# Kernel tuning notes

Measured on AMD Instinct MI355X. Metric: run time of the kernel, lower is better.

The kernel has to match this reference:

```python
import jax, jax.numpy as jnp
import numpy as np

N, K, CL, CP = 8192, 32, 384, 128   # residues, neighbours, local dim, pair dim
H, S, P = 4, 32, 8                   # heads, head size, query points


def setup_inputs() -> dict:
    key = jax.random.key(0)
    ks = jax.random.split(key, 12)

    def lin(k, fi, fo):
        return jax.random.normal(k, (fi, fo), jnp.float32) / jnp.sqrt(jnp.float32(fi))

    return {
        "local": jax.random.normal(ks[0], (N, CL), jnp.float32),
        "pair": jax.random.normal(ks[1], (N, K, CP), jnp.float32),
        "frames": jax.random.normal(ks[2], (N, 4, 4), jnp.float32),
        "neighbours": jax.random.randint(ks[3], (N, K), 0, N),
        "mask": jnp.ones((N, K), dtype=bool),
        "Wq": lin(ks[4], CL, H * S), "bq": jnp.zeros((H * S,), jnp.float32),
        "Wk": lin(ks[5], CL, S), "bk": jnp.zeros((S,), jnp.float32),
        "Wv": lin(ks[6], CL, S), "bv": jnp.zeros((S,), jnp.float32),
        "Wqp": lin(ks[7], CL, H * P * 3), "bqp": jnp.zeros((H * P * 3,), jnp.float32),
        "Wkp": lin(ks[8], CL, P * 3), "bkp": jnp.zeros((P * 3,), jnp.float32),
        "Wvp": lin(ks[9], CL, P * 3), "bvp": jnp.zeros((P * 3,), jnp.float32),
        "Wb": lin(ks[10], CP, H),
        "gamma": jnp.full((H,), np.log(np.exp(1.0) - 1.0), jnp.float32),
        "Wout": lin(ks[11], H * S + H * CP + H * P * 3, CL),
    }


def _ln(x):
    # hk.LayerNorm([-1], create_scale=False, create_offset=False), eps=1e-5
    m = x.mean(-1, keepdims=True)
    v = ((x - m) ** 2).mean(-1, keepdims=True)
    return (x - m) * jax.lax.rsqrt(v + 1e-5)


def reference(local, pair, frames, neighbours, mask,
              Wq, bq, Wk, bk, Wv, bv, Wqp, bqp, Wkp, bkp, Wvp, bvp,
              Wb, gamma, Wout):
    frames = frames.astype(jnp.float32)
    rot = frames[:, :3, :3]       # (N,3,3)
    trans = frames[:, :3, 3]      # (N,3)
    n = local.shape[0]

    q = _ln((local @ Wq + bq).reshape(n, H, S))   # (N,H,S)
    k = _ln(local @ Wk + bk)                      # (N,S)  single (shared) head
    v = local @ Wv + bv                           # (N,S)

    def pts(W, b, h):
        p = (local @ W + b).reshape(n, h, P, 3)
        # frames[:,None,None].apply_to_point: rot @ p + trans
        return jnp.einsum('nab,nhpb->nhpa', rot, p) + trans[:, None, None, :]

    qp = pts(Wqp, bqp, H)            # (N,H,P,3)
    kp = pts(Wkp, bkp, 1)[:, 0]      # (N,P,3)
    vp = pts(Wvp, bvp, 1)[:, 0]      # (N,P,3)

    w_C = jnp.sqrt(2.0 / (9.0 * P))
    w_L = jnp.sqrt(1.0 / 3.0)
    scale = jax.nn.softplus(gamma)[None, None, :] * w_C / 2   # (1,1,H)

    logits = jnp.einsum('nhc,nkc->nkh', q / jnp.sqrt(jnp.float32(S)), k[neighbours])
    diff = qp[:, None] - kp[neighbours][:, :, None]           # (N,K,H,P,3)
    dist = (diff ** 2).sum((-1, -2))                          # (N,K,H)
    logits = w_L * (logits - scale * dist + pair @ Wb)
    logits = jnp.where(mask[..., None], logits, -1e9)
    attn = jax.nn.softmax(logits, axis=1)
    attn = jnp.where(mask[..., None], attn, 0)

    local_up = jnp.einsum('nkh,nkc->nhc', attn, v[neighbours]).reshape(n, -1)
    pair_up = jnp.einsum('nkh,nkc->nhc', attn, pair).reshape(n, -1)
    pt = jnp.einsum('nkh,nkpa->nhpa', attn, vp[neighbours])   # (N,H,P,3)
    # apply_inverse_to_point: rot^T @ (x - trans)
    pt = jnp.einsum('nba,nhpb->nhpa', rot, pt - trans[:, None, None, :])

    result = jnp.concatenate([local_up, pair_up, pt.reshape(n, -1)], axis=-1)
    return result @ Wout
```

## Files before the change

### kernel.cpp

```cpp
#include <hip/hip_runtime.h>
#include <hip/hip_bf16.h>

#define NN 8192
#define KK 32
#define CL 384
#define CP 128
#define HH 4
#define SS 32
#define PP 8
#define PW 336
#define RW 736

__global__ void pack_weights(const float* __restrict__ Wq, const float* __restrict__ Wk,
                             const float* __restrict__ Wv, const float* __restrict__ Wqp,
                             const float* __restrict__ Wkp, const float* __restrict__ Wvp,
                             const float* __restrict__ bq, const float* __restrict__ bk,
                             const float* __restrict__ bv, const float* __restrict__ bqp,
                             const float* __restrict__ bkp, const float* __restrict__ bvp,
                             float* __restrict__ W_all, float* __restrict__ b_all) {
  int c = blockIdx.x;
  for (int j = threadIdx.x; j < PW; j += blockDim.x) {
    float w;
    if (j < 128)      w = Wq[c*128 + j];
    else if (j < 160) w = Wk[c*32 + (j-128)];
    else if (j < 192) w = Wv[c*32 + (j-160)];
    else if (j < 288) w = Wqp[c*96 + (j-192)];
    else if (j < 312) w = Wkp[c*24 + (j-288)];
    else              w = Wvp[c*24 + (j-312)];
    W_all[c*PW + j] = w;
    if (c == 0) {
      float b;
      if (j < 128)      b = bq[j];
      else if (j < 160) b = bk[j-128];
      else if (j < 192) b = bv[j-160];
      else if (j < 288) b = bqp[j-192];
      else if (j < 312) b = bkp[j-288];
      else              b = bvp[j-312];
      b_all[j] = b;
    }
  }
}

template<bool BIAS>
__global__ __launch_bounds__(256, 4) void gemm_f32(
    const float* __restrict__ A, const float* __restrict__ B,
    const float* __restrict__ bias, float* __restrict__ C,
    int M, int Kd, int Nc) {
  constexpr int BM = 64, BN = 64, BK = 32;
  __shared__ float As[BK][BM + 4];
  __shared__ float Bs[BK][BN + 4];
  int tid = threadIdx.x;
  int tx = tid & 15, ty = tid >> 4;
  int m0 = blockIdx.y * BM, n0 = blockIdx.x * BN;
  float acc[4][4] = {};
  for (int k0 = 0; k0 < Kd; k0 += BK) {
    int arow = tid >> 3, achunk = tid & 7;
#pragma unroll
    for (int half = 0; half < 2; ++half) {
      int m = arow + half * 32;
      float4 v = *(const float4*)(A + (size_t)(m0 + m) * Kd + k0 + achunk * 4);
      As[achunk*4+0][m] = v.x; As[achunk*4+1][m] = v.y;
      As[achunk*4+2][m] = v.z; As[achunk*4+3][m] = v.w;
    }
    int bc4 = tid & 15, br = tid >> 4;
#pragma unroll
    for (int half = 0; half < 2; ++half) {
      int kk = br + half * 16;
      float4 v = make_float4(0.f, 0.f, 0.f, 0.f);
      if (n0 + bc4 * 4 < Nc)
        v = *(const float4*)(B + (size_t)(k0 + kk) * Nc + n0 + bc4 * 4);
      *(float4*)&Bs[kk][bc4 * 4] = v;
    }
    __syncthreads();
#pragma unroll
    for (int kk = 0; kk < BK; ++kk) {
      float a[4], b[4];
      *(float4*)&a[0] = *(const float4*)&As[kk][ty * 4];
      *(float4*)&b[0] = *(const float4*)&Bs[kk][tx * 4];
#pragma unroll
      for (int i = 0; i < 4; ++i)
#pragma unroll
        for (int jj = 0; jj < 4; ++jj)
          acc[i][jj] += a[i] * b[jj];
    }
    __syncthreads();
  }
#pragma unroll
  for (int i = 0; i < 4; ++i) {
    int rowi = m0 + ty * 4 + i;
    int col = n0 + tx * 4;
    if (col + 3 < Nc) {
      float4 v;
      v.x = acc[i][0]; v.y = acc[i][1]; v.z = acc[i][2]; v.w = acc[i][3];
      if (BIAS) { v.x += bias[col]; v.y += bias[col+1]; v.z += bias[col+2]; v.w += bias[col+3]; }
      *(float4*)(C + (size_t)rowi * Nc + col) = v;
    } else {
      for (int jj = 0; jj < 4; ++jj) {
        int cc = col + jj;
        if (cc < Nc) C[(size_t)rowi * Nc + cc] = acc[i][jj] + (BIAS ? bias[cc] : 0.f);
      }
    }
  }
}

__global__ __launch_bounds__(256) void transform_kernel(
    const float* __restrict__ proj, const float* __restrict__ frames,
    float* __restrict__ feats) {
  int lane = threadIdx.x & 63;
  int node = blockIdx.x * 4 + (threadIdx.x >> 6);
  const float* pr = proj + (size_t)node * PW;
  float* fr = feats + (size_t)node * PW;
  const float* F = frames + (size_t)node * 16;
  int j = lane & 31;
#pragma unroll
  for (int pass = 0; pass < 2; ++pass) {
    int h = pass * 2 + (lane >> 5);
    float x = pr[h * 32 + j];
    float s = x;
#pragma unroll
    for (int m = 16; m >= 1; m >>= 1) s += __shfl_xor(s, m, 32);
    float mean = s * (1.f / 32.f);
    float d = x - mean;
    float vs = d * d;
#pragma unroll
    for (int m = 16; m >= 1; m >>= 1) vs += __shfl_xor(vs, m, 32);
    fr[h * 32 + j] = d / sqrtf(vs * (1.f / 32.f) + 1e-5f);
  }
  if (lane < 32) {
    float x = pr[128 + j];
    float s = x;
#pragma unroll
    for (int m = 16; m >= 1; m >>= 1) s += __shfl_xor(s, m, 32);
    float mean = s * (1.f / 32.f);
    float d = x - mean;
    float vs = d * d;
#pragma unroll
    for (int m = 16; m >= 1; m >>= 1) vs += __shfl_xor(vs, m, 32);
    fr[128 + j] = d / sqrtf(vs * (1.f / 32.f) + 1e-5f);
  } else {
    fr[160 + j] = pr[160 + j];
  }
  if (lane < 48) {
    int c = 192 + lane * 3;
    float x = pr[c], y = pr[c + 1], z = pr[c + 2];
#pragma unroll
    for (int a = 0; a < 3; ++a)
      fr[c + a] = F[a*4+0]*x + F[a*4+1]*y + F[a*4+2]*z + F[a*4+3];
  }
}

__global__ __launch_bounds__(256) void attn_kernel(
    const float* __restrict__ feats, const float* __restrict__ pair,
    const int* __restrict__ neighbours, const float* __restrict__ frames,
    const float* __restrict__ Wb, const float* __restrict__ gamma,
    float* __restrict__ result) {
  int n = blockIdx.x;
  int tid = threadIdx.x;
  __shared__ float qT_s[128];
  __shared__ float qp_s[96];
  __shared__ int   nb_s[32];
  __shared__ float kv_s[32][68];
  __shared__ float kpvp_s[32][52];
  __shared__ float pair_s[32][132];
  __shared__ float Wb_s[512];
  __shared__ float logit_s[32][4];
  __shared__ float attn_s[32][4];
  __shared__ float mred[4], sred[4];
  __shared__ float pt_s[96];

  const float* fr = feats + (size_t)n * PW;
  if (tid < 128) qT_s[(tid & 31) * 4 + (tid >> 5)] = fr[tid];
  if (tid < 96) qp_s[tid] = fr[192 + tid];
  if (tid < 32) nb_s[tid] = neighbours[n * KK + tid];
  Wb_s[tid] = Wb[tid];
  Wb_s[tid + 256] = Wb[tid + 256];
  __syncthreads();

  {
    int k = tid >> 3, r = tid & 7;
    const float* src = feats + (size_t)nb_s[k] * PW;
    float4 v0 = *(const float4*)(src + 128 + r * 8);
    float4 v1 = *(const float4*)(src + 128 + r * 8 + 4);
    *(float4*)&kv_s[k][r * 8] = v0;
    *(float4*)&kv_s[k][r * 8 + 4] = v1;
#pragma unroll
    for (int i = 0; i < 6; ++i) kpvp_s[k][r * 6 + i] = src[288 + r * 6 + i];
  }
  {
    const float* psrc = pair + (size_t)n * (KK * CP);
    for (int t = tid; t < 1024; t += 256) {
      int row = t >> 5, c4 = t & 31;
      float4 v = *(const float4*)(psrc + row * 128 + c4 * 4);
      *(float4*)&pair_s[row][c4 * 4] = v;
    }
  }
  __syncthreads();

  if (tid < 128) {
    int k = tid >> 2, h = tid & 3;
    float qk = 0.f;
#pragma unroll
    for (int c = 0; c < 32; ++c) qk += qT_s[c * 4 + h] * kv_s[k][c];
    float dist = 0.f;
#pragma unroll
    for (int r = 0; r < 24; ++r) {
      float d = qp_s[h * 24 + r] - kpvp_s[k][r];
      dist += d * d;
    }
    float bias = 0.f;
    for (int c = 0; c < 128; ++c) bias += pair_s[k][c] * Wb_s[c * 4 + h];
    float scale = log1pf(expf(gamma[h])) * (1.f / 6.f) * 0.5f;
    const float wL = 0.57735026918962576f;
    logit_s[k][h] = wL * (qk * 0.17677669529663687f - scale * dist + bias);
  }
  __syncthreads();
  if (tid < 4) {
    float m = -1e30f;
    for (int k = 0; k < 32; ++k) m = fmaxf(m, logit_s[k][tid]);
    float s = 0.f;
    for (int k = 0; k < 32; ++k) s += expf(logit_s[k][tid] - m);
    mred[tid] = m;
    sred[tid] = 1.f / s;
  }
  __syncthreads();
  if (tid < 128) {
    int k = tid >> 2, h = tid & 3;
    attn_s[k][h] = expf(logit_s[k][h] - mred[h]) * sred[h];
  }
  __syncthreads();

  float* out = result + (size_t)n * RW;
  if (tid < 128) {
    int h = tid >> 5, c = tid & 31;
    float s = 0.f;
#pragma unroll
    for (int k = 0; k < 32; ++k) s += attn_s[k][h] * kv_s[k][32 + c];
    out[h * 32 + c] = s;
  }
  if (tid < 96) {
    int h = tid / 24, r = tid % 24;
    float s = 0.f;
#pragma unroll
    for (int k = 0; k < 32; ++k) s += attn_s[k][h] * kpvp_s[k][24 + r];
    pt_s[tid] = s;
  }
#pragma unroll
  for (int half = 0; half < 2; ++half) {
    int idx = tid + half * 256;
    int h = idx >> 7, c = idx & 127;
    float s = 0.f;
#pragma unroll
    for (int k = 0; k < 32; ++k) s += attn_s[k][h] * pair_s[k][c];
    out[128 + h * 128 + c] = s;
  }
  __syncthreads();
  if (tid < 96) {
    int h = tid / 24, p = (tid % 24) / 3, a = tid % 3;
    const float* F = frames + (size_t)n * 16;
    float s = 0.f;
#pragma unroll
    for (int b = 0; b < 3; ++b)
      s += F[b * 4 + a] * (pt_s[h * 24 + p * 3 + b] - F[b * 4 + 3]);
    out[640 + tid] = s;
  }
}

extern "C" void kernel_launch(void* const* d_in, const int* in_sizes, int n_in,
                              void* d_out, int out_size, void* d_ws, size_t ws_size,
                              hipStream_t stream) {
  (void)in_sizes; (void)n_in; (void)out_size; (void)ws_size;
  const float* local      = (const float*)d_in[0];
  const float* pair       = (const float*)d_in[1];
  const float* frames     = (const float*)d_in[2];
  const int*   neighbours = (const int*)d_in[3];
  const float* Wq   = (const float*)d_in[5];
  const float* bq   = (const float*)d_in[6];
  const float* Wk   = (const float*)d_in[7];
  const float* bk   = (const float*)d_in[8];
  const float* Wv   = (const float*)d_in[9];
  const float* bv   = (const float*)d_in[10];
  const float* Wqp  = (const float*)d_in[11];
  const float* bqp  = (const float*)d_in[12];
  const float* Wkp  = (const float*)d_in[13];
  const float* bkp  = (const float*)d_in[14];
  const float* Wvp  = (const float*)d_in[15];
  const float* bvp  = (const float*)d_in[16];
  const float* Wb   = (const float*)d_in[17];
  const float* gamma= (const float*)d_in[18];
  const float* Wout = (const float*)d_in[19];

  float* ws     = (float*)d_ws;
  float* W_all  = ws;
  float* b_all  = W_all + 384 * PW;
  float* proj   = b_all + PW;
  float* feats  = proj + (size_t)NN * PW;
  float* result = feats + (size_t)NN * PW;
  float* out    = (float*)d_out;

  hipLaunchKernelGGL(pack_weights, dim3(CL), dim3(256), 0, stream,
                     Wq, Wk, Wv, Wqp, Wkp, Wvp, bq, bk, bv, bqp, bkp, bvp, W_all, b_all);
  hipLaunchKernelGGL((gemm_f32<true>), dim3((PW + 63) / 64, NN / 64), dim3(256), 0, stream,
                     local, W_all, b_all, proj, NN, CL, PW);
  hipLaunchKernelGGL(transform_kernel, dim3(NN / 4), dim3(256), 0, stream,
                     proj, frames, feats);
  hipLaunchKernelGGL(attn_kernel, dim3(NN), dim3(256), 0, stream,
                     feats, pair, neighbours, frames, Wb, gamma, result);
  hipLaunchKernelGGL((gemm_f32<false>), dim3(CL / 64, NN / 64), dim3(256), 0, stream,
                     result, Wout, nullptr, out, NN, RW, CL);
}
```

Before: 412.0 us.

## Restructure projection GEMM and per-residue attention kernel for more parallelism

```diff
diff --git a/kernel.cpp b/kernel.cpp
--- a/kernel.cpp
+++ b/kernel.cpp
@@ -10,6 +10,8 @@
 #define PP 8
 #define PW 336
 #define RW 736
+
+#define FMA4(ac, s, b) { (ac).x += (s)*(b).x; (ac).y += (s)*(b).y; (ac).z += (s)*(b).z; (ac).w += (s)*(b).w; }
 
 __global__ void pack_weights(const float* __restrict__ Wq, const float* __restrict__ Wk,
                              const float* __restrict__ Wv, const float* __restrict__ Wqp,
@@ -42,63 +44,86 @@
 }
 
 template<bool BIAS>
-__global__ __launch_bounds__(256, 4) void gemm_f32(
+__global__ __launch_bounds__(128) void gemm_f32(
     const float* __restrict__ A, const float* __restrict__ B,
     const float* __restrict__ bias, float* __restrict__ C,
     int M, int Kd, int Nc) {
-  constexpr int BM = 64, BN = 64, BK = 32;
-  __shared__ float As[BK][BM + 4];
-  __shared__ float Bs[BK][BN + 4];
-  int tid = threadIdx.x;
-  int tx = tid & 15, ty = tid >> 4;
-  int m0 = blockIdx.y * BM, n0 = blockIdx.x * BN;
-  float acc[4][4] = {};
-  for (int k0 = 0; k0 < Kd; k0 += BK) {
-    int arow = tid >> 3, achunk = tid & 7;
-#pragma unroll
-    for (int half = 0; half < 2; ++half) {
-      int m = arow + half * 32;
-      float4 v = *(const float4*)(A + (size_t)(m0 + m) * Kd + k0 + achunk * 4);
-      As[achunk*4+0][m] = v.x; As[achunk*4+1][m] = v.y;
-      As[achunk*4+2][m] = v.z; As[achunk*4+3][m] = v.w;
-    }
-    int bc4 = tid & 15, br = tid >> 4;
-#pragma unroll
-    for (int half = 0; half < 2; ++half) {
-      int kk = br + half * 16;
-      float4 v = make_float4(0.f, 0.f, 0.f, 0.f);
-      if (n0 + bc4 * 4 < Nc)
-        v = *(const float4*)(B + (size_t)(k0 + kk) * Nc + n0 + bc4 * 4);
-      *(float4*)&Bs[kk][bc4 * 4] = v;
+  constexpr int BK = 32;
+  __shared__ float As[BK * 68];
+  __shared__ float Bs[BK * 68];
+  const int tid = threadIdx.x;
+  const int tx = tid & 15, ty = tid >> 4;
+  const int m0 = blockIdx.y * 64, n0 = blockIdx.x * 64;
+  const int achunk = tid & 7;
+  const int arow0 = tid >> 3;
+  const int bc4 = tid & 15;
+  const int brow0 = tid >> 4;
+  const int bcol = n0 + bc4 * 4;
+  const bool bok = (bcol + 3) < Nc;
+
+  float4 rA[4], rB[4];
+  const int NT = Kd / BK;
+
+  {
+#pragma unroll
+    for (int u = 0; u < 4; ++u)
+      rA[u] = *(const float4*)(A + (size_t)(m0 + arow0 + u * 16) * Kd + achunk * 4);
+#pragma unroll
+    for (int u = 0; u < 4; ++u)
+      rB[u] = bok ? *(const float4*)(B + (size_t)(brow0 + u * 8) * Nc + bcol)
+                  : make_float4(0.f, 0.f, 0.f, 0.f);
+  }
+
+  float4 acc[8];
+#pragma unroll
+  for (int i = 0; i < 8; ++i) acc[i] = make_float4(0.f, 0.f, 0.f, 0.f);
+
+  for (int t = 0; t < NT; ++t) {
+#pragma unroll
+    for (int u = 0; u < 4; ++u) {
+      int m = arow0 + u * 16;
+      As[(achunk * 4 + 0) * 68 + m] = rA[u].x;
+      As[(achunk * 4 + 1) * 68 + m] = rA[u].y;
+      As[(achunk * 4 + 2) * 68 + m] = rA[u].z;
+      As[(achunk * 4 + 3) * 68 + m] = rA[u].w;
+      *(float4*)&Bs[(brow0 + u * 8) * 68 + bc4 * 4] = rB[u];
     }
     __syncthreads();
+    if (t + 1 < NT) {
+      int k0 = (t + 1) * BK;
+#pragma unroll
+      for (int u = 0; u < 4; ++u)
+        rA[u] = *(const float4*)(A + (size_t)(m0 + arow0 + u * 16) * Kd + k0 + achunk * 4);
+#pragma unroll
+      for (int u = 0; u < 4; ++u)
+        rB[u] = bok ? *(const float4*)(B + (size_t)(k0 + brow0 + u * 8) * Nc + bcol)
+                    : make_float4(0.f, 0.f, 0.f, 0.f);
+    }
 #pragma unroll
     for (int kk = 0; kk < BK; ++kk) {
-      float a[4], b[4];
-      *(float4*)&a[0] = *(const float4*)&As[kk][ty * 4];
-      *(float4*)&b[0] = *(const float4*)&Bs[kk][tx * 4];
-#pragma unroll
-      for (int i = 0; i < 4; ++i)
-#pragma unroll
-        for (int jj = 0; jj < 4; ++jj)
-          acc[i][jj] += a[i] * b[jj];
+      float4 a0 = *(const float4*)&As[kk * 68 + ty * 8];
+      float4 a1 = *(const float4*)&As[kk * 68 + ty * 8 + 4];
+      float4 b  = *(const float4*)&Bs[kk * 68 + tx * 4];
+      FMA4(acc[0], a0.x, b); FMA4(acc[1], a0.y, b);
+      FMA4(acc[2], a0.z, b); FMA4(acc[3], a0.w, b);
+      FMA4(acc[4], a1.x, b); FMA4(acc[5], a1.y, b);
+      FMA4(acc[6], a1.z, b); FMA4(acc[7], a1.w, b);
     }
     __syncthreads();
   }
-#pragma unroll
-  for (int i = 0; i < 4; ++i) {
-    int rowi = m0 + ty * 4 + i;
-    int col = n0 + tx * 4;
-    if (col + 3 < Nc) {
-      float4 v;
-      v.x = acc[i][0]; v.y = acc[i][1]; v.z = acc[i][2]; v.w = acc[i][3];
-      if (BIAS) { v.x += bias[col]; v.y += bias[col+1]; v.z += bias[col+2]; v.w += bias[col+3]; }
-      *(float4*)(C + (size_t)rowi * Nc + col) = v;
-    } else {
-      for (int jj = 0; jj < 4; ++jj) {
-        int cc = col + jj;
-        if (cc < Nc) C[(size_t)rowi * Nc + cc] = acc[i][jj] + (BIAS ? bias[cc] : 0.f);
-      }
+
+  if (bok) {
+    float4 bv = make_float4(0.f, 0.f, 0.f, 0.f);
+    if (BIAS) {
+      bv.x = bias[bcol]; bv.y = bias[bcol + 1];
+      bv.z = bias[bcol + 2]; bv.w = bias[bcol + 3];
+    }
+#pragma unroll
+    for (int i = 0; i < 8; ++i) {
+      int row = m0 + ty * 8 + i;
+      float4 v = acc[i];
+      if (BIAS) { v.x += bv.x; v.y += bv.y; v.z += bv.z; v.w += bv.w; }
+      *(float4*)(C + (size_t)row * Nc + bcol) = v;
     }
   }
 }
@@ -154,113 +179,152 @@
     const int* __restrict__ neighbours, const float* __restrict__ frames,
     const float* __restrict__ Wb, const float* __restrict__ gamma,
     float* __restrict__ result) {
-  int n = blockIdx.x;
-  int tid = threadIdx.x;
-  __shared__ float qT_s[128];
+  const int n = blockIdx.x;
+  const int tid = threadIdx.x;
+  __shared__ float q_s[4 * 36];
   __shared__ float qp_s[96];
-  __shared__ int   nb_s[32];
-  __shared__ float kv_s[32][68];
-  __shared__ float kpvp_s[32][52];
-  __shared__ float pair_s[32][132];
-  __shared__ float Wb_s[512];
-  __shared__ float logit_s[32][4];
-  __shared__ float attn_s[32][4];
-  __shared__ float mred[4], sred[4];
+  __shared__ float kv_s[32 * 68];
+  __shared__ float kpvp_s[32 * 52];
+  __shared__ float pair_s[32 * 140];
+  __shared__ float bias_s[128];
+  __shared__ float attn_s[128];
+  __shared__ float red_s[16], red2_s[16];
   __shared__ float pt_s[96];
 
   const float* fr = feats + (size_t)n * PW;
-  if (tid < 128) qT_s[(tid & 31) * 4 + (tid >> 5)] = fr[tid];
-  if (tid < 96) qp_s[tid] = fr[192 + tid];
-  if (tid < 32) nb_s[tid] = neighbours[n * KK + tid];
-  Wb_s[tid] = Wb[tid];
-  Wb_s[tid + 256] = Wb[tid + 256];
-  __syncthreads();
-
+  float* out = result + (size_t)n * RW;
+
+  if (tid < 128) q_s[(tid >> 5) * 36 + (tid & 31)] = fr[tid];
+  else if (tid < 224) qp_s[tid - 128] = fr[192 + (tid - 128)];
   {
-    int k = tid >> 3, r = tid & 7;
-    const float* src = feats + (size_t)nb_s[k] * PW;
+    const int k = tid >> 3, r = tid & 7;
+    const int nbk = neighbours[n * KK + k];
+    const float* src = feats + (size_t)nbk * PW;
     float4 v0 = *(const float4*)(src + 128 + r * 8);
     float4 v1 = *(const float4*)(src + 128 + r * 8 + 4);
-    *(float4*)&kv_s[k][r * 8] = v0;
-    *(float4*)&kv_s[k][r * 8 + 4] = v1;
-#pragma unroll
-    for (int i = 0; i < 6; ++i) kpvp_s[k][r * 6 + i] = src[288 + r * 6 + i];
-  }
+    *(float4*)&kv_s[k * 68 + r * 8] = v0;
+    *(float4*)&kv_s[k * 68 + r * 8 + 4] = v1;
+#pragma unroll
+    for (int i = 0; i < 6; ++i) kpvp_s[k * 52 + r * 6 + i] = src[288 + r * 6 + i];
+    const float* psrc = pair + (size_t)n * (KK * CP);
+#pragma unroll
+    for (int it = 0; it < 4; ++it) {
+      int t = tid + it * 256;
+      int row = t >> 5, c4 = t & 31;
+      *(float4*)&pair_s[row * 140 + c4 * 4] = *(const float4*)(psrc + row * 128 + c4 * 4);
+    }
+  }
+  __syncthreads();
+
   {
-    const float* psrc = pair + (size_t)n * (KK * CP);
-    for (int t = tid; t < 1024; t += 256) {
-      int row = t >> 5, c4 = t & 31;
-      float4 v = *(const float4*)(psrc + row * 128 + c4 * 4);
-      *(float4*)&pair_s[row][c4 * 4] = v;
-    }
+    const int k = tid >> 3, r = tid & 7;
+    float4 p0 = *(const float4*)&pair_s[k * 140 + r * 16];
+    float4 p1 = *(const float4*)&pair_s[k * 140 + r * 16 + 4];
+    float4 p2 = *(const float4*)&pair_s[k * 140 + r * 16 + 8];
+    float4 p3 = *(const float4*)&pair_s[k * 140 + r * 16 + 12];
+    float pv[16] = {p0.x,p0.y,p0.z,p0.w, p1.x,p1.y,p1.z,p1.w,
+                    p2.x,p2.y,p2.z,p2.w, p3.x,p3.y,p3.z,p3.w};
+    const float4* Wb4 = (const float4*)Wb;
+    float4 b4 = make_float4(0.f, 0.f, 0.f, 0.f);
+#pragma unroll
+    for (int i = 0; i < 16; ++i) {
+      float4 w = Wb4[r * 16 + i];
+      FMA4(b4, pv[i], w);
+    }
+#pragma unroll
+    for (int m = 1; m <= 4; m <<= 1) {
+      b4.x += __shfl_xor(b4.x, m);
+      b4.y += __shfl_xor(b4.y, m);
+      b4.z += __shfl_xor(b4.z, m);
+      b4.w += __shfl_xor(b4.w, m);
+    }
+    if (r == 0) *(float4*)&bias_s[k * 4] = b4;
   }
   __syncthreads();
 
+  {
+    const int lk = tid >> 3, lh = (tid >> 1) & 3, le = tid & 1;
+    float qk = 0.f;
+#pragma unroll
+    for (int j = 0; j < 4; ++j) {
+      float4 qv = *(const float4*)&q_s[lh * 36 + le * 16 + j * 4];
+      float4 kv = *(const float4*)&kv_s[lk * 68 + le * 16 + j * 4];
+      qk += qv.x*kv.x + qv.y*kv.y + qv.z*kv.z + qv.w*kv.w;
+    }
+    float dist = 0.f;
+#pragma unroll
+    for (int j = 0; j < 3; ++j) {
+      float4 qpv = *(const float4*)&qp_s[lh * 24 + le * 12 + j * 4];
+      float4 kpv = *(const float4*)&kpvp_s[lk * 52 + le * 12 + j * 4];
+      float d0 = qpv.x - kpv.x, d1 = qpv.y - kpv.y;
+      float d2 = qpv.z - kpv.z, d3 = qpv.w - kpv.w;
+      dist += d0*d0 + d1*d1 + d2*d2 + d3*d3;
+    }
+    float scale = log1pf(__expf(gamma[lh])) * (1.f / 12.f);
+    float part = qk * 0.17677669529663687f - scale * dist;
+    part += __shfl_xor(part, 1);
+    float logit = 0.57735026918962576f * (part + bias_s[lk * 4 + lh]);
+    float mw = logit;
+#pragma unroll
+    for (int m = 8; m <= 32; m <<= 1) mw = fmaxf(mw, __shfl_xor(mw, m));
+    const int w = tid >> 6;
+    if ((tid & 63) == lh * 2) red_s[w * 4 + lh] = mw;
+    __syncthreads();
+    float mx = fmaxf(fmaxf(red_s[lh], red_s[4 + lh]),
+                     fmaxf(red_s[8 + lh], red_s[12 + lh]));
+    float p = __expf(logit - mx);
+    float sw = p;
+#pragma unroll
+    for (int m = 8; m <= 32; m <<= 1) sw += __shfl_xor(sw, m);
+    if ((tid & 63) == lh * 2) red2_s[w * 4 + lh] = sw;
+    __syncthreads();
+    float denom = red2_s[lh] + red2_s[4 + lh] + red2_s[8 + lh] + red2_s[12 + lh];
+    if (le == 0) attn_s[lk * 4 + lh] = p / denom;
+  }
+  __syncthreads();
+
   if (tid < 128) {
-    int k = tid >> 2, h = tid & 3;
-    float qk = 0.f;
-#pragma unroll
-    for (int c = 0; c < 32; ++c) qk += qT_s[c * 4 + h] * kv_s[k][c];
-    float dist = 0.f;
-#pragma unroll
-    for (int r = 0; r < 24; ++r) {
-      float d = qp_s[h * 24 + r] - kpvp_s[k][r];
-      dist += d * d;
-    }
-    float bias = 0.f;
-    for (int c = 0; c < 128; ++c) bias += pair_s[k][c] * Wb_s[c * 4 + h];
-    float scale = log1pf(expf(gamma[h])) * (1.f / 6.f) * 0.5f;
-    const float wL = 0.57735026918962576f;
-    logit_s[k][h] = wL * (qk * 0.17677669529663687f - scale * dist + bias);
+    const int h = tid >> 5, c4 = (tid & 31) * 4;
+    float4 acc = make_float4(0.f, 0.f, 0.f, 0.f);
+#pragma unroll
+    for (int k = 0; k < 32; ++k) {
+      float av = attn_s[k * 4 + h];
+      float4 pv = *(const float4*)&pair_s[k * 140 + c4];
+      FMA4(acc, av, pv);
+    }
+    *(float4*)(out + 128 + h * 128 + c4) = acc;
+  } else if (tid < 160) {
+    const int idx = tid - 128;
+    const int h = idx >> 3, c4 = (idx & 7) * 4;
+    float4 acc = make_float4(0.f, 0.f, 0.f, 0.f);
+#pragma unroll
+    for (int k = 0; k < 32; ++k) {
+      float av = attn_s[k * 4 + h];
+      float4 vv = *(const float4*)&kv_s[k * 68 + 32 + c4];
+      FMA4(acc, av, vv);
+    }
+    *(float4*)(out + h * 32 + c4) = acc;
+  } else if (tid < 184) {
+    const int idx = tid - 160;
+    const int h = idx / 6, q6 = (idx % 6) * 4;
+    float4 acc = make_float4(0.f, 0.f, 0.f, 0.f);
+#pragma unroll
+    for (int k = 0; k < 32; ++k) {
+      float av = attn_s[k * 4 + h];
+      float4 vv = *(const float4*)&kpvp_s[k * 52 + 24 + q6];
+      FMA4(acc, av, vv);
+    }
+    *(float4*)&pt_s[h * 24 + q6] = acc;
   }
   __syncthreads();
-  if (tid < 4) {
-    float m = -1e30f;
-    for (int k = 0; k < 32; ++k) m = fmaxf(m, logit_s[k][tid]);
-    float s = 0.f;
-    for (int k = 0; k < 32; ++k) s += expf(logit_s[k][tid] - m);
-    mred[tid] = m;
-    sred[tid] = 1.f / s;
-  }
-  __syncthreads();
-  if (tid < 128) {
-    int k = tid >> 2, h = tid & 3;
-    attn_s[k][h] = expf(logit_s[k][h] - mred[h]) * sred[h];
-  }
-  __syncthreads();
-
-  float* out = result + (size_t)n * RW;
-  if (tid < 128) {
-    int h = tid >> 5, c = tid & 31;
-    float s = 0.f;
-#pragma unroll
-    for (int k = 0; k < 32; ++k) s += attn_s[k][h] * kv_s[k][32 + c];
-    out[h * 32 + c] = s;
-  }
+
   if (tid < 96) {
-    int h = tid / 24, r = tid % 24;
-    float s = 0.f;
-#pragma unroll
-    for (int k = 0; k < 32; ++k) s += attn_s[k][h] * kpvp_s[k][24 + r];
-    pt_s[tid] = s;
-  }
-#pragma unroll
-  for (int half = 0; half < 2; ++half) {
-    int idx = tid + half * 256;
-    int h = idx >> 7, c = idx & 127;
-    float s = 0.f;
-#pragma unroll
-    for (int k = 0; k < 32; ++k) s += attn_s[k][h] * pair_s[k][c];
-    out[128 + h * 128 + c] = s;
-  }
-  __syncthreads();
-  if (tid < 96) {
-    int h = tid / 24, p = (tid % 24) / 3, a = tid % 3;
+    const int h = tid / 24, rr = tid % 24, pp = rr / 3, aa = rr % 3;
     const float* F = frames + (size_t)n * 16;
     float s = 0.f;
 #pragma unroll
     for (int b = 0; b < 3; ++b)
-      s += F[b * 4 + a] * (pt_s[h * 24 + p * 3 + b] - F[b * 4 + 3]);
+      s += F[b * 4 + aa] * (pt_s[h * 24 + pp * 3 + b] - F[b * 4 + 3]);
     out[640 + tid] = s;
   }
 }
@@ -299,12 +363,12 @@
 
   hipLaunchKernelGGL(pack_weights, dim3(CL), dim3(256), 0, stream,
                      Wq, Wk, Wv, Wqp, Wkp, Wvp, bq, bk, bv, bqp, bkp, bvp, W_all, b_all);
-  hipLaunchKernelGGL((gemm_f32<true>), dim3((PW + 63) / 64, NN / 64), dim3(256), 0, stream,
+  hipLaunchKernelGGL((gemm_f32<true>), dim3((PW + 63) / 64, NN / 64), dim3(128), 0, stream,
                      local, W_all, b_all, proj, NN, CL, PW);
   hipLaunchKernelGGL(transform_kernel, dim3(NN / 4), dim3(256), 0, stream,
                      proj, frames, feats);
   hipLaunchKernelGGL(attn_kernel, dim3(NN), dim3(256), 0, stream,
                      feats, pair, neighbours, frames, Wb, gamma, result);
-  hipLaunchKernelGGL((gemm_f32<false>), dim3(CL / 64, NN / 64), dim3(256), 0, stream,
+  hipLaunchKernelGGL((gemm_f32<false>), dim3(CL / 64, NN / 64), dim3(128), 0, stream,
                      result, Wout, nullptr, out, NN, RW, CL);
 }
```

After: 490.9 us. +19.1%, slower.
